# Kernel optimization log

Measured on AMD Instinct MI355X. Metric: run time of the kernel, lower is better.

## Reference

```python
import jax, jax.numpy as jnp
import numpy as np

WEIGHT_THRESH = 0.5
EPS = 1e-5


def setup_inputs() -> dict:
    key = jax.random.key(0)
    k1, k2, k3 = jax.random.split(key, 3)
    B, N = 2048, 4096
    src_points = jax.random.normal(k1, (B, N, 3), dtype=jnp.float32)
    tgt_points = jax.random.normal(k2, (B, N, 3), dtype=jnp.float32)
    weights = jax.random.uniform(k3, (B, N), dtype=jnp.float32)
    return {"src_points": src_points, "tgt_points": tgt_points, "weights": weights}


def reference(src_points, tgt_points, weights):
    # threshold + normalize weights  (B, N)
    w = jnp.where(weights < WEIGHT_THRESH, jnp.zeros_like(weights), weights)
    w = w / (jnp.sum(w, axis=1, keepdims=True) + EPS)
    w = w[:, :, None]  # (B, N, 1)

    # weighted centroids (B, 1, 3)
    src_centroid = jnp.sum(src_points * w, axis=1, keepdims=True)
    ref_centroid = jnp.sum(tgt_points * w, axis=1, keepdims=True)

    src_c = src_points - src_centroid
    ref_c = tgt_points - ref_centroid

    # weighted 3x3 covariance H = src_c^T @ (ref_c * w)   (B, 3, 3)
    H = jnp.einsum('bni,bnj->bij', src_c, ref_c * w)

    # Kabsch: tf.linalg.svd returns S, U, V (V not transposed); jnp returns U, S, Vh
    U, S, Vh = jnp.linalg.svd(H)
    V = jnp.swapaxes(Vh, -1, -2)
    Ut = jnp.swapaxes(U, -1, -2)
    det = jnp.linalg.det(jnp.matmul(V, Ut))  # (B,)

    ones = jnp.ones_like(det)
    d = jnp.stack([ones, ones, jnp.sign(det)], axis=-1)  # (B, 3) diag of sign-fix eye
    R = jnp.matmul(V * d[:, None, :], Ut)  # V @ diag(d) @ U^T  (B, 3, 3)

    t = ref_centroid[:, 0, :] - jnp.einsum('bij,bj->bi', R, src_centroid[:, 0, :])  # (B, 3)
    return R, t
```

## Files before the change

### kernel.cpp

```cpp
#include <hip/hip_runtime.h>
#include <math.h>

#define BATCH   2048
#define NPTS    4096
#define THREADS 256
#define CHUNKS  4
#define CPTS    (NPTS / CHUNKS)
#define WTHRESH 0.5f
#define EPS     1e-5

__device__ __forceinline__ void accumulate4(const float* __restrict__ sb,
                                            const float* __restrict__ tb,
                                            const float* __restrict__ wb,
                                            float* acc) {
  const int p0 = threadIdx.x * 4;
  float4 w4 = *(const float4*)(wb + p0);
  const float4* sp = (const float4*)(sb + (size_t)p0 * 3);
  float4 s0 = sp[0], s1 = sp[1], s2 = sp[2];
  const float4* tp = (const float4*)(tb + (size_t)p0 * 3);
  float4 r0 = tp[0], r1 = tp[1], r2 = tp[2];

  float ww[4] = {w4.x, w4.y, w4.z, w4.w};
  float ps[4][3] = {{s0.x, s0.y, s0.z}, {s0.w, s1.x, s1.y},
                    {s1.z, s1.w, s2.x}, {s2.y, s2.z, s2.w}};
  float qs[4][3] = {{r0.x, r0.y, r0.z}, {r0.w, r1.x, r1.y},
                    {r1.z, r1.w, r2.x}, {r2.y, r2.z, r2.w}};
#pragma unroll
  for (int i = 0; i < 16; ++i) acc[i] = 0.f;
#pragma unroll
  for (int i = 0; i < 4; ++i) {
    float w = (ww[i] < WTHRESH) ? 0.f : ww[i];
    acc[0] += w;
    float wp0 = w * ps[i][0], wp1 = w * ps[i][1], wp2 = w * ps[i][2];
    acc[1] += wp0; acc[2] += wp1; acc[3] += wp2;
    acc[4] += w * qs[i][0]; acc[5] += w * qs[i][1]; acc[6] += w * qs[i][2];
    acc[7]  += wp0 * qs[i][0]; acc[8]  += wp0 * qs[i][1]; acc[9]  += wp0 * qs[i][2];
    acc[10] += wp1 * qs[i][0]; acc[11] += wp1 * qs[i][1]; acc[12] += wp1 * qs[i][2];
    acc[13] += wp2 * qs[i][0]; acc[14] += wp2 * qs[i][1]; acc[15] += wp2 * qs[i][2];
  }
}

__device__ __forceinline__ void reduce_block16(float* acc, float* red ) {
#pragma unroll
  for (int off = 32; off > 0; off >>= 1) {
#pragma unroll
    for (int i = 0; i < 16; ++i) acc[i] += __shfl_down(acc[i], off, 64);
  }
  const int wave = threadIdx.x >> 6;
  const int lane = threadIdx.x & 63;
  if (lane == 0) {
#pragma unroll
    for (int i = 0; i < 16; ++i) red[wave * 16 + i] = acc[i];
  }
  __syncthreads();
  if (threadIdx.x == 0) {
#pragma unroll
    for (int w = 1; w < 4; ++w)
#pragma unroll
      for (int i = 0; i < 16; ++i) acc[i] += red[w * 16 + i];
  }
}

__device__ void solve_from_acc(const float* acc, float* R9, float* t3) {
  double W = acc[0];
  double inv = 1.0 / (W + EPS);
  double sc[3], tc[3];
#pragma unroll
  for (int i = 0; i < 3; ++i) { sc[i] = (double)acc[1 + i] * inv; tc[i] = (double)acc[4 + i] * inv; }
  double ssum = W * inv;

  double H[3][3];
#pragma unroll
  for (int i = 0; i < 3; ++i)
#pragma unroll
    for (int j = 0; j < 3; ++j)
      H[i][j] = (double)acc[7 + 3 * i + j] * inv - sc[i] * tc[j] * (2.0 - ssum);

  double A[3][3];
#pragma unroll
  for (int i = 0; i < 3; ++i)
#pragma unroll
    for (int j = 0; j < 3; ++j)
      A[i][j] = H[0][i] * H[0][j] + H[1][i] * H[1][j] + H[2][i] * H[2][j];

  double V[3][3] = {{1, 0, 0}, {0, 1, 0}, {0, 0, 1}};

  const int PQ[3][2] = {{0, 1}, {0, 2}, {1, 2}};
  for (int sweep = 0; sweep < 8; ++sweep) {
    double off = fabs(A[0][1]) + fabs(A[0][2]) + fabs(A[1][2]);
    if (off < 1e-26) break;
#pragma unroll
    for (int r = 0; r < 3; ++r) {
      int p = PQ[r][0], q = PQ[r][1];
      double apq = A[p][q];
      if (fabs(apq) < 1e-300) continue;
      double theta = (A[q][q] - A[p][p]) / (2.0 * apq);
      double tj = copysign(1.0, theta) / (fabs(theta) + sqrt(theta * theta + 1.0));
      double c = 1.0 / sqrt(tj * tj + 1.0);
      double sn = tj * c;
#pragma unroll
      for (int k = 0; k < 3; ++k) {
        double akp = A[k][p], akq = A[k][q];
        A[k][p] = c * akp - sn * akq;
        A[k][q] = sn * akp + c * akq;
      }
#pragma unroll
      for (int k = 0; k < 3; ++k) {
        double apk = A[p][k], aqk = A[q][k];
        A[p][k] = c * apk - sn * aqk;
        A[q][k] = sn * apk + c * aqk;
      }
#pragma unroll
      for (int k = 0; k < 3; ++k) {
        double vkp = V[k][p], vkq = V[k][q];
        V[k][p] = c * vkp - sn * vkq;
        V[k][q] = sn * vkp + c * vkq;
      }
    }
  }

  double e[3] = {A[0][0], A[1][1], A[2][2]};
  int i0 = 0, i1 = 1, i2 = 2, tswap;
  if (e[i0] < e[i1]) { tswap = i0; i0 = i1; i1 = tswap; }
  if (e[i0] < e[i2]) { tswap = i0; i0 = i2; i2 = tswap; }
  if (e[i1] < e[i2]) { tswap = i1; i1 = i2; i2 = tswap; }

  double v1[3], v2[3], v3[3];
#pragma unroll
  for (int k = 0; k < 3; ++k) { v1[k] = V[k][i0]; v2[k] = V[k][i1]; v3[k] = V[k][i2]; }

  double u1[3], u2[3];
#pragma unroll
  for (int k = 0; k < 3; ++k) u1[k] = H[k][0] * v1[0] + H[k][1] * v1[1] + H[k][2] * v1[2];
  double n1 = sqrt(u1[0] * u1[0] + u1[1] * u1[1] + u1[2] * u1[2]);
  if (n1 > 1e-150) { double r = 1.0 / n1; u1[0] *= r; u1[1] *= r; u1[2] *= r; }
  else { u1[0] = 1.0; u1[1] = 0.0; u1[2] = 0.0; }

#pragma unroll
  for (int k = 0; k < 3; ++k) u2[k] = H[k][0] * v2[0] + H[k][1] * v2[1] + H[k][2] * v2[2];
  double d12 = u1[0] * u2[0] + u1[1] * u2[1] + u1[2] * u2[2];
#pragma unroll
  for (int k = 0; k < 3; ++k) u2[k] -= d12 * u1[k];
  double n2 = sqrt(u2[0] * u2[0] + u2[1] * u2[1] + u2[2] * u2[2]);
  if (n2 > 1e-150) { double r = 1.0 / n2; u2[0] *= r; u2[1] *= r; u2[2] *= r; }
  else {
    double ax = fabs(u1[0]);
    double t0 = (ax < 0.9) ? 1.0 : 0.0, t1v = (ax < 0.9) ? 0.0 : 1.0;
    u2[0] = t0 - (t0 * u1[0] + t1v * u1[1]) * u1[0];
    u2[1] = t1v - (t0 * u1[0] + t1v * u1[1]) * u1[1];
    u2[2] = -(t0 * u1[0] + t1v * u1[1]) * u1[2];
    double nn = sqrt(u2[0] * u2[0] + u2[1] * u2[1] + u2[2] * u2[2]);
    u2[0] /= nn; u2[1] /= nn; u2[2] /= nn;
  }

  double w3[3] = {u1[1] * u2[2] - u1[2] * u2[1],
                  u1[2] * u2[0] - u1[0] * u2[2],
                  u1[0] * u2[1] - u1[1] * u2[0]};

  double cx = v2[1] * v3[2] - v2[2] * v3[1];
  double cy = v2[2] * v3[0] - v2[0] * v3[2];
  double cz = v2[0] * v3[1] - v2[1] * v3[0];
  double detV = v1[0] * cx + v1[1] * cy + v1[2] * cz;
  detV = (detV >= 0.0) ? 1.0 : -1.0;

  double R[3][3];
#pragma unroll
  for (int i = 0; i < 3; ++i)
#pragma unroll
    for (int j = 0; j < 3; ++j)
      R[i][j] = v1[i] * u1[j] + v2[i] * u2[j] + detV * v3[i] * w3[j];

#pragma unroll
  for (int i = 0; i < 3; ++i) {
#pragma unroll
    for (int j = 0; j < 3; ++j) R9[3 * i + j] = (float)R[i][j];
    t3[i] = (float)(tc[i] - (R[i][0] * sc[0] + R[i][1] * sc[1] + R[i][2] * sc[2]));
  }
}

__global__ __launch_bounds__(THREADS) void wp_reduce_split(const float* __restrict__ src,
                                                           const float* __restrict__ tgt,
                                                           const float* __restrict__ wts,
                                                           float* __restrict__ partials) {
  __shared__ float red[64];
  const int bid = blockIdx.x;
  const int b = bid >> 2;
  const int c = bid & 3;
  const size_t off = (size_t)b * NPTS + (size_t)c * CPTS;
  float acc[16];
  accumulate4(src + off * 3, tgt + off * 3, wts + off, acc);
  reduce_block16(acc, red);
  if (threadIdx.x == 0) {
#pragma unroll
    for (int i = 0; i < 16; ++i) partials[(size_t)bid * 16 + i] = acc[i];
  }
}

__global__ __launch_bounds__(64) void wp_solve(const float* __restrict__ partials,
                                               float* __restrict__ out) {
  const int b = blockIdx.x * 64 + threadIdx.x;
  if (b >= BATCH) return;
  float acc[16];
#pragma unroll
  for (int i = 0; i < 16; ++i) acc[i] = 0.f;
#pragma unroll
  for (int cch = 0; cch < CHUNKS; ++cch)
#pragma unroll
    for (int i = 0; i < 16; ++i)
      acc[i] += partials[(size_t)(b * CHUNKS + cch) * 16 + i];
  float R9[9], t3[3];
  solve_from_acc(acc, R9, t3);
#pragma unroll
  for (int i = 0; i < 9; ++i) out[(size_t)b * 9 + i] = R9[i];
#pragma unroll
  for (int i = 0; i < 3; ++i) out[(size_t)BATCH * 9 + (size_t)b * 3 + i] = t3[i];
}

__global__ __launch_bounds__(THREADS) void wp_fused(const float* __restrict__ src,
                                                    const float* __restrict__ tgt,
                                                    const float* __restrict__ wts,
                                                    float* __restrict__ out) {
  __shared__ float red[64];
  const int b = blockIdx.x;
  float accT[16];
  float acc[16];
#pragma unroll
  for (int i = 0; i < 16; ++i) acc[i] = 0.f;
  for (int c = 0; c < CHUNKS; ++c) {
    const size_t off = (size_t)b * NPTS + (size_t)c * CPTS;
    accumulate4(src + off * 3, tgt + off * 3, wts + off, accT);
#pragma unroll
    for (int i = 0; i < 16; ++i) acc[i] += accT[i];
  }
  reduce_block16(acc, red);
  if (threadIdx.x == 0) {
    float R9[9], t3[3];
    solve_from_acc(acc, R9, t3);
#pragma unroll
    for (int i = 0; i < 9; ++i) out[(size_t)b * 9 + i] = R9[i];
#pragma unroll
    for (int i = 0; i < 3; ++i) out[(size_t)BATCH * 9 + (size_t)b * 3 + i] = t3[i];
  }
}

extern "C" void kernel_launch(void* const* d_in, const int* in_sizes, int n_in,
                              void* d_out, int out_size, void* d_ws, size_t ws_size,
                              hipStream_t stream) {
  const float* src = (const float*)d_in[0];
  const float* tgt = (const float*)d_in[1];
  const float* wts = (const float*)d_in[2];
  float* out = (float*)d_out;

  if (ws_size >= (size_t)BATCH * CHUNKS * 16 * sizeof(float)) {
    float* partials = (float*)d_ws;
    wp_reduce_split<<<BATCH * CHUNKS, THREADS, 0, stream>>>(src, tgt, wts, partials);
    wp_solve<<<(BATCH + 63) / 64, 64, 0, stream>>>(partials, out);
  } else {
    wp_fused<<<BATCH, THREADS, 0, stream>>>(src, tgt, wts, out);
  }
}
```

Baseline: 243.6 us.

## Stage point loads through LDS with async global_load_lds and unroll Jacobi solver

The reduction kernel now brings its chunk of weights, source and target points into shared memory with direct global-to-LDS async loads that move fully coalesced 16-byte pieces, then each thread reads its 4 points from LDS. Before, each thread did strided float4 global loads. The 3x3 solve is rewritten into scalar, branch-free Jacobi rotations with a fixed 7 sweeps and no early exit, plus select-based sorting, to reduce divergence. The cost is extra LDS traffic, more LDS per block (which may reduce occupancy), and always running the full set of sweeps.

```diff
diff --git a/kernel.cpp b/kernel.cpp
--- a/kernel.cpp
+++ b/kernel.cpp
@@ -9,24 +9,39 @@
 #define WTHRESH 0.5f
 #define EPS     1e-5
 
-__device__ __forceinline__ void accumulate4(const float* __restrict__ sb,
-                                            const float* __restrict__ tb,
-                                            const float* __restrict__ wb,
-                                            float* acc) {
-  const int p0 = threadIdx.x * 4;
-  float4 w4 = *(const float4*)(wb + p0);
-  const float4* sp = (const float4*)(sb + (size_t)p0 * 3);
-  float4 s0 = sp[0], s1 = sp[1], s2 = sp[2];
-  const float4* tp = (const float4*)(tb + (size_t)p0 * 3);
-  float4 r0 = tp[0], r1 = tp[1], r2 = tp[2];
-
+__device__ __forceinline__ void async_ld16(const void* g, void* l) {
+  __builtin_amdgcn_global_load_lds((const __attribute__((address_space(1))) void*)g,
+                                   (__attribute__((address_space(3))) void*)l, 16, 0, 0);
+}
+
+__device__ __forceinline__ void reduce_block16(float* acc, float* red ) {
+#pragma unroll
+  for (int off = 32; off > 0; off >>= 1) {
+#pragma unroll
+    for (int i = 0; i < 16; ++i) acc[i] += __shfl_down(acc[i], off, 64);
+  }
+  const int wave = threadIdx.x >> 6;
+  const int lane = threadIdx.x & 63;
+  if (lane == 0) {
+#pragma unroll
+    for (int i = 0; i < 16; ++i) red[wave * 16 + i] = acc[i];
+  }
+  __syncthreads();
+  if (threadIdx.x == 0) {
+#pragma unroll
+    for (int w = 1; w < 4; ++w)
+#pragma unroll
+      for (int i = 0; i < 16; ++i) acc[i] += red[w * 16 + i];
+  }
+}
+
+__device__ __forceinline__ void accum_pts(float4 w4, float4 s0, float4 s1, float4 s2,
+                                          float4 r0, float4 r1, float4 r2, float* acc) {
   float ww[4] = {w4.x, w4.y, w4.z, w4.w};
   float ps[4][3] = {{s0.x, s0.y, s0.z}, {s0.w, s1.x, s1.y},
                     {s1.z, s1.w, s2.x}, {s2.y, s2.z, s2.w}};
   float qs[4][3] = {{r0.x, r0.y, r0.z}, {r0.w, r1.x, r1.y},
                     {r1.z, r1.w, r2.x}, {r2.y, r2.z, r2.w}};
-#pragma unroll
-  for (int i = 0; i < 16; ++i) acc[i] = 0.f;
 #pragma unroll
   for (int i = 0; i < 4; ++i) {
     float w = (ww[i] < WTHRESH) ? 0.f : ww[i];
@@ -40,157 +55,166 @@
   }
 }
 
-__device__ __forceinline__ void reduce_block16(float* acc, float* red ) {
-#pragma unroll
-  for (int off = 32; off > 0; off >>= 1) {
-#pragma unroll
-    for (int i = 0; i < 16; ++i) acc[i] += __shfl_down(acc[i], off, 64);
-  }
-  const int wave = threadIdx.x >> 6;
-  const int lane = threadIdx.x & 63;
-  if (lane == 0) {
-#pragma unroll
-    for (int i = 0; i < 16; ++i) red[wave * 16 + i] = acc[i];
-  }
-  __syncthreads();
-  if (threadIdx.x == 0) {
-#pragma unroll
-    for (int w = 1; w < 4; ++w)
-#pragma unroll
-      for (int i = 0; i < 16; ++i) acc[i] += red[w * 16 + i];
-  }
-}
+
+#define JROT(app, aqq, apq, apt, aqt, vp0, vq0, vp1, vq1, vp2, vq2)            \
+  {                                                                            \
+    bool go = fabs(apq) > 1e-300;                                              \
+    double apq_s = go ? apq : 1.0;                                             \
+    double theta = (aqq - app) / (2.0 * apq_s);                                \
+    double tt = copysign(1.0, theta) / (fabs(theta) + sqrt(theta*theta + 1.0));\
+    double cc = 1.0 / sqrt(tt*tt + 1.0);                                       \
+    double ss = tt * cc;                                                       \
+    cc = go ? cc : 1.0; ss = go ? ss : 0.0;                                    \
+    double app_n = cc*cc*app - 2.0*cc*ss*apq + ss*ss*aqq;                      \
+    double aqq_n = ss*ss*app + 2.0*cc*ss*apq + cc*cc*aqq;                      \
+    double apt_n = cc*apt - ss*aqt;                                            \
+    double aqt_n = ss*apt + cc*aqt;                                            \
+    app = app_n; aqq = aqq_n; apq = 0.0; apt = apt_n; aqt = aqt_n;             \
+    double tv;                                                                 \
+    tv = vp0; vp0 = cc*tv - ss*vq0; vq0 = ss*tv + cc*vq0;                      \
+    tv = vp1; vp1 = cc*tv - ss*vq1; vq1 = ss*tv + cc*vq1;                      \
+    tv = vp2; vp2 = cc*tv - ss*vq2; vq2 = ss*tv + cc*vq2;                      \
+  }
+
+#define CSWAP(ea, eb, x0, y0, x1, y1, x2, y2)                                  \
+  { bool sw = ea < eb; double td;                                              \
+    td = ea; ea = sw ? eb : ea; eb = sw ? td : eb;                             \
+    td = x0; x0 = sw ? y0 : x0; y0 = sw ? td : y0;                             \
+    td = x1; x1 = sw ? y1 : x1; y1 = sw ? td : y1;                             \
+    td = x2; x2 = sw ? y2 : x2; y2 = sw ? td : y2; }
 
 __device__ void solve_from_acc(const float* acc, float* R9, float* t3) {
-  double W = acc[0];
-  double inv = 1.0 / (W + EPS);
-  double sc[3], tc[3];
-#pragma unroll
-  for (int i = 0; i < 3; ++i) { sc[i] = (double)acc[1 + i] * inv; tc[i] = (double)acc[4 + i] * inv; }
-  double ssum = W * inv;
-
-  double H[3][3];
-#pragma unroll
-  for (int i = 0; i < 3; ++i)
-#pragma unroll
-    for (int j = 0; j < 3; ++j)
-      H[i][j] = (double)acc[7 + 3 * i + j] * inv - sc[i] * tc[j] * (2.0 - ssum);
-
-  double A[3][3];
-#pragma unroll
-  for (int i = 0; i < 3; ++i)
-#pragma unroll
-    for (int j = 0; j < 3; ++j)
-      A[i][j] = H[0][i] * H[0][j] + H[1][i] * H[1][j] + H[2][i] * H[2][j];
-
-  double V[3][3] = {{1, 0, 0}, {0, 1, 0}, {0, 0, 1}};
-
-  const int PQ[3][2] = {{0, 1}, {0, 2}, {1, 2}};
-  for (int sweep = 0; sweep < 8; ++sweep) {
-    double off = fabs(A[0][1]) + fabs(A[0][2]) + fabs(A[1][2]);
-    if (off < 1e-26) break;
-#pragma unroll
-    for (int r = 0; r < 3; ++r) {
-      int p = PQ[r][0], q = PQ[r][1];
-      double apq = A[p][q];
-      if (fabs(apq) < 1e-300) continue;
-      double theta = (A[q][q] - A[p][p]) / (2.0 * apq);
-      double tj = copysign(1.0, theta) / (fabs(theta) + sqrt(theta * theta + 1.0));
-      double c = 1.0 / sqrt(tj * tj + 1.0);
-      double sn = tj * c;
-#pragma unroll
-      for (int k = 0; k < 3; ++k) {
-        double akp = A[k][p], akq = A[k][q];
-        A[k][p] = c * akp - sn * akq;
-        A[k][q] = sn * akp + c * akq;
-      }
-#pragma unroll
-      for (int k = 0; k < 3; ++k) {
-        double apk = A[p][k], aqk = A[q][k];
-        A[p][k] = c * apk - sn * aqk;
-        A[q][k] = sn * apk + c * aqk;
-      }
-#pragma unroll
-      for (int k = 0; k < 3; ++k) {
-        double vkp = V[k][p], vkq = V[k][q];
-        V[k][p] = c * vkp - sn * vkq;
-        V[k][q] = sn * vkp + c * vkq;
-      }
-    }
-  }
-
-  double e[3] = {A[0][0], A[1][1], A[2][2]};
-  int i0 = 0, i1 = 1, i2 = 2, tswap;
-  if (e[i0] < e[i1]) { tswap = i0; i0 = i1; i1 = tswap; }
-  if (e[i0] < e[i2]) { tswap = i0; i0 = i2; i2 = tswap; }
-  if (e[i1] < e[i2]) { tswap = i1; i1 = i2; i2 = tswap; }
-
-  double v1[3], v2[3], v3[3];
-#pragma unroll
-  for (int k = 0; k < 3; ++k) { v1[k] = V[k][i0]; v2[k] = V[k][i1]; v3[k] = V[k][i2]; }
-
-  double u1[3], u2[3];
-#pragma unroll
-  for (int k = 0; k < 3; ++k) u1[k] = H[k][0] * v1[0] + H[k][1] * v1[1] + H[k][2] * v1[2];
-  double n1 = sqrt(u1[0] * u1[0] + u1[1] * u1[1] + u1[2] * u1[2]);
-  if (n1 > 1e-150) { double r = 1.0 / n1; u1[0] *= r; u1[1] *= r; u1[2] *= r; }
-  else { u1[0] = 1.0; u1[1] = 0.0; u1[2] = 0.0; }
-
-#pragma unroll
-  for (int k = 0; k < 3; ++k) u2[k] = H[k][0] * v2[0] + H[k][1] * v2[1] + H[k][2] * v2[2];
-  double d12 = u1[0] * u2[0] + u1[1] * u2[1] + u1[2] * u2[2];
-#pragma unroll
-  for (int k = 0; k < 3; ++k) u2[k] -= d12 * u1[k];
-  double n2 = sqrt(u2[0] * u2[0] + u2[1] * u2[1] + u2[2] * u2[2]);
-  if (n2 > 1e-150) { double r = 1.0 / n2; u2[0] *= r; u2[1] *= r; u2[2] *= r; }
-  else {
-    double ax = fabs(u1[0]);
-    double t0 = (ax < 0.9) ? 1.0 : 0.0, t1v = (ax < 0.9) ? 0.0 : 1.0;
-    u2[0] = t0 - (t0 * u1[0] + t1v * u1[1]) * u1[0];
-    u2[1] = t1v - (t0 * u1[0] + t1v * u1[1]) * u1[1];
-    u2[2] = -(t0 * u1[0] + t1v * u1[1]) * u1[2];
-    double nn = sqrt(u2[0] * u2[0] + u2[1] * u2[1] + u2[2] * u2[2]);
-    u2[0] /= nn; u2[1] /= nn; u2[2] /= nn;
-  }
-
-  double w3[3] = {u1[1] * u2[2] - u1[2] * u2[1],
-                  u1[2] * u2[0] - u1[0] * u2[2],
-                  u1[0] * u2[1] - u1[1] * u2[0]};
-
-  double cx = v2[1] * v3[2] - v2[2] * v3[1];
-  double cy = v2[2] * v3[0] - v2[0] * v3[2];
-  double cz = v2[0] * v3[1] - v2[1] * v3[0];
-  double detV = v1[0] * cx + v1[1] * cy + v1[2] * cz;
-  detV = (detV >= 0.0) ? 1.0 : -1.0;
-
-  double R[3][3];
-#pragma unroll
-  for (int i = 0; i < 3; ++i)
-#pragma unroll
-    for (int j = 0; j < 3; ++j)
-      R[i][j] = v1[i] * u1[j] + v2[i] * u2[j] + detV * v3[i] * w3[j];
-
-#pragma unroll
-  for (int i = 0; i < 3; ++i) {
-#pragma unroll
-    for (int j = 0; j < 3; ++j) R9[3 * i + j] = (float)R[i][j];
-    t3[i] = (float)(tc[i] - (R[i][0] * sc[0] + R[i][1] * sc[1] + R[i][2] * sc[2]));
-  }
-}
-
-__global__ __launch_bounds__(THREADS) void wp_reduce_split(const float* __restrict__ src,
-                                                           const float* __restrict__ tgt,
-                                                           const float* __restrict__ wts,
-                                                           float* __restrict__ partials) {
+  const double W = acc[0];
+  const double inv = 1.0 / (W + EPS);
+  const double sc0 = acc[1] * inv, sc1 = acc[2] * inv, sc2 = acc[3] * inv;
+  const double tc0 = acc[4] * inv, tc1 = acc[5] * inv, tc2 = acc[6] * inv;
+  const double f = 2.0 - W * inv;
+
+  const double h00 = acc[7]  * inv - sc0 * tc0 * f;
+  const double h01 = acc[8]  * inv - sc0 * tc1 * f;
+  const double h02 = acc[9]  * inv - sc0 * tc2 * f;
+  const double h10 = acc[10] * inv - sc1 * tc0 * f;
+  const double h11 = acc[11] * inv - sc1 * tc1 * f;
+  const double h12 = acc[12] * inv - sc1 * tc2 * f;
+  const double h20 = acc[13] * inv - sc2 * tc0 * f;
+  const double h21 = acc[14] * inv - sc2 * tc1 * f;
+  const double h22 = acc[15] * inv - sc2 * tc2 * f;
+
+  double a00 = h00*h00 + h10*h10 + h20*h20;
+  double a01 = h00*h01 + h10*h11 + h20*h21;
+  double a02 = h00*h02 + h10*h12 + h20*h22;
+  double a11 = h01*h01 + h11*h11 + h21*h21;
+  double a12 = h01*h02 + h11*h12 + h21*h22;
+  double a22 = h02*h02 + h12*h12 + h22*h22;
+
+  double v00 = 1, v01 = 0, v02 = 0;
+  double v10 = 0, v11 = 1, v12 = 0;
+  double v20 = 0, v21 = 0, v22 = 1;
+
+  for (int sweep = 0; sweep < 7; ++sweep) {
+    JROT(a00, a11, a01, a02, a12, v00, v01, v10, v11, v20, v21)
+    JROT(a00, a22, a02, a01, a12, v00, v02, v10, v12, v20, v22)
+    JROT(a11, a22, a12, a01, a02, v01, v02, v11, v12, v21, v22)
+  }
+
+  double e0 = a00, e1 = a11, e2 = a22;
+  CSWAP(e0, e1, v00, v01, v10, v11, v20, v21)
+  CSWAP(e0, e2, v00, v02, v10, v12, v20, v22)
+  CSWAP(e1, e2, v01, v02, v11, v12, v21, v22)
+
+  double u1x = h00*v00 + h01*v10 + h02*v20;
+  double u1y = h10*v00 + h11*v10 + h12*v20;
+  double u1z = h20*v00 + h21*v10 + h22*v20;
+  double n1 = sqrt(u1x*u1x + u1y*u1y + u1z*u1z);
+  bool ok1 = n1 > 1e-150;
+  double r1 = 1.0 / n1;
+  u1x = ok1 ? u1x * r1 : 1.0;
+  u1y = ok1 ? u1y * r1 : 0.0;
+  u1z = ok1 ? u1z * r1 : 0.0;
+
+  double u2x = h00*v01 + h01*v11 + h02*v21;
+  double u2y = h10*v01 + h11*v11 + h12*v21;
+  double u2z = h20*v01 + h21*v11 + h22*v21;
+  double d12 = u1x*u2x + u1y*u2y + u1z*u2z;
+  u2x -= d12 * u1x; u2y -= d12 * u1y; u2z -= d12 * u1z;
+  double n2 = sqrt(u2x*u2x + u2y*u2y + u2z*u2z);
+  bool ok2 = n2 > 1e-150;
+  double fx = (fabs(u1x) < 0.9) ? 1.0 : 0.0;
+  double fy = 1.0 - fx;
+  double dd = fx*u1x + fy*u1y;
+  double gx = fx - dd*u1x, gy = fy - dd*u1y, gz = -dd*u1z;
+  double rg = 1.0 / sqrt(gx*gx + gy*gy + gz*gz);
+  double r2 = 1.0 / n2;
+  u2x = ok2 ? u2x * r2 : gx * rg;
+  u2y = ok2 ? u2y * r2 : gy * rg;
+  u2z = ok2 ? u2z * r2 : gz * rg;
+
+  double w3x = u1y*u2z - u1z*u2y;
+  double w3y = u1z*u2x - u1x*u2z;
+  double w3z = u1x*u2y - u1y*u2x;
+
+  double cxx = v11*v22 - v21*v12;
+  double cxy = v21*v02 - v01*v22;
+  double cxz = v01*v12 - v11*v02;
+  double dv = v00*cxx + v10*cxy + v20*cxz;
+  dv = (dv >= 0.0) ? 1.0 : -1.0;
+
+  double R00 = v00*u1x + v01*u2x + dv*v02*w3x;
+  double R01 = v00*u1y + v01*u2y + dv*v02*w3y;
+  double R02 = v00*u1z + v01*u2z + dv*v02*w3z;
+  double R10 = v10*u1x + v11*u2x + dv*v12*w3x;
+  double R11 = v10*u1y + v11*u2y + dv*v12*w3y;
+  double R12 = v10*u1z + v11*u2z + dv*v12*w3z;
+  double R20 = v20*u1x + v21*u2x + dv*v22*w3x;
+  double R21 = v20*u1y + v21*u2y + dv*v22*w3y;
+  double R22 = v20*u1z + v21*u2z + dv*v22*w3z;
+
+  R9[0] = (float)R00; R9[1] = (float)R01; R9[2] = (float)R02;
+  R9[3] = (float)R10; R9[4] = (float)R11; R9[5] = (float)R12;
+  R9[6] = (float)R20; R9[7] = (float)R21; R9[8] = (float)R22;
+  t3[0] = (float)(tc0 - (R00*sc0 + R01*sc1 + R02*sc2));
+  t3[1] = (float)(tc1 - (R10*sc0 + R11*sc1 + R12*sc2));
+  t3[2] = (float)(tc2 - (R20*sc0 + R21*sc1 + R22*sc2));
+}
+
+__global__ __launch_bounds__(THREADS) void wp_reduce_lds(const float* __restrict__ src,
+                                                         const float* __restrict__ tgt,
+                                                         const float* __restrict__ wts,
+                                                         float* __restrict__ partials) {
+  __shared__ float4 lds_w[CPTS / 4];
+  __shared__ float4 lds_s[CPTS * 3 / 4];
+  __shared__ float4 lds_t[CPTS * 3 / 4];
   __shared__ float red[64];
+
   const int bid = blockIdx.x;
   const int b = bid >> 2;
   const int c = bid & 3;
-  const size_t off = (size_t)b * NPTS + (size_t)c * CPTS;
+  const size_t poff = (size_t)b * NPTS + (size_t)c * CPTS;
+  const float4* gw = (const float4*)(wts + poff);
+  const float4* gs = (const float4*)(src + poff * 3);
+  const float4* gt = (const float4*)(tgt + poff * 3);
+
+  const int t = threadIdx.x;
+  async_ld16(gw + t, lds_w + t);
+#pragma unroll
+  for (int k = 0; k < 3; ++k) async_ld16(gs + t + k * THREADS, lds_s + t + k * THREADS);
+#pragma unroll
+  for (int k = 0; k < 3; ++k) async_ld16(gt + t + k * THREADS, lds_t + t + k * THREADS);
+
+  asm volatile("s_waitcnt vmcnt(0)" ::: "memory");
+  __syncthreads();
+
+  float4 w4 = lds_w[t];
+  float4 s0 = lds_s[t * 3], s1 = lds_s[t * 3 + 1], s2 = lds_s[t * 3 + 2];
+  float4 r0 = lds_t[t * 3], r1 = lds_t[t * 3 + 1], r2 = lds_t[t * 3 + 2];
+
   float acc[16];
-  accumulate4(src + off * 3, tgt + off * 3, wts + off, acc);
+#pragma unroll
+  for (int i = 0; i < 16; ++i) acc[i] = 0.f;
+  accum_pts(w4, s0, s1, s2, r0, r1, r2, acc);
+
   reduce_block16(acc, red);
-  if (threadIdx.x == 0) {
+  if (t == 0) {
 #pragma unroll
     for (int i = 0; i < 16; ++i) partials[(size_t)bid * 16 + i] = acc[i];
   }
@@ -222,15 +246,16 @@
                                                     float* __restrict__ out) {
   __shared__ float red[64];
   const int b = blockIdx.x;
-  float accT[16];
   float acc[16];
 #pragma unroll
   for (int i = 0; i < 16; ++i) acc[i] = 0.f;
   for (int c = 0; c < CHUNKS; ++c) {
-    const size_t off = (size_t)b * NPTS + (size_t)c * CPTS;
-    accumulate4(src + off * 3, tgt + off * 3, wts + off, accT);
-#pragma unroll
-    for (int i = 0; i < 16; ++i) acc[i] += accT[i];
+    const size_t poff = (size_t)b * NPTS + (size_t)c * CPTS;
+    const int p0 = threadIdx.x * 4;
+    float4 w4 = *(const float4*)(wts + poff + p0);
+    const float4* sp = (const float4*)(src + (poff + p0) * 3);
+    const float4* tp = (const float4*)(tgt + (poff + p0) * 3);
+    accum_pts(w4, sp[0], sp[1], sp[2], tp[0], tp[1], tp[2], acc);
   }
   reduce_block16(acc, red);
   if (threadIdx.x == 0) {
@@ -253,7 +278,7 @@
 
   if (ws_size >= (size_t)BATCH * CHUNKS * 16 * sizeof(float)) {
     float* partials = (float*)d_ws;
-    wp_reduce_split<<<BATCH * CHUNKS, THREADS, 0, stream>>>(src, tgt, wts, partials);
+    wp_reduce_lds<<<BATCH * CHUNKS, THREADS, 0, stream>>>(src, tgt, wts, partials);
     wp_solve<<<(BATCH + 63) / 64, 64, 0, stream>>>(partials, out);
   } else {
     wp_fused<<<BATCH, THREADS, 0, stream>>>(src, tgt, wts, out);
```

After: 245.3 us. About the same (+0.7%).
